# Optimization experiments

Hardware: AMD Instinct MI355X
Metric: run time of the kernel (lower is better)

## Reference

```python
import jax, jax.numpy as jnp
import numpy as np

T, B, I, H, O_FREQ, O_CTX = 1024, 32, 64, 1024, 64, 8
ALPHA = 0.1  # leak rate
G = 1.5      # chaotic gain used by init_weights


def setup_inputs() -> dict:
    key = jax.random.key(0)
    ks = jax.random.split(key, 8)
    std1 = G / np.sqrt(H)  # init_weights scaling

    def centered_normal(k, shape, std):
        w = jax.random.normal(k, shape, dtype=jnp.float32)
        return (w - w.mean()) * std

    input_sig = jax.random.normal(ks[0], (T, B, I), dtype=jnp.float32)
    rate = jax.random.uniform(ks[1], (B, H), dtype=jnp.float32, minval=-1.0, maxval=1.0)
    i2h_w = centered_normal(ks[2], (H, I), std1)
    i2h_b = jnp.zeros((H,), dtype=jnp.float32)
    h2h_w = centered_normal(ks[3], (H, H), std1)
    h2h_b = jnp.zeros((H,), dtype=jnp.float32)
    h2o_w = centered_normal(ks[4], (O_FREQ, H), std1)
    h2o_b = jnp.zeros((O_FREQ,), dtype=jnp.float32)
    h2o_ctx_w = jax.random.normal(ks[5], (O_CTX, H), dtype=jnp.float32)
    h2o_ctx_b = jnp.zeros((O_CTX,), dtype=jnp.float32)
    return {
        "input_sig": input_sig, "rate": rate,
        "i2h_w": i2h_w, "i2h_b": i2h_b,
        "h2h_w": h2h_w, "h2h_b": h2h_b,
        "h2o_w": h2o_w, "h2o_b": h2o_b,
        "h2o_ctx_w": h2o_ctx_w, "h2o_ctx_b": h2o_ctx_b,
    }


def reference(input_sig, rate, i2h_w, i2h_b, h2h_w, h2h_b,
              h2o_w, h2o_b, h2o_ctx_w, h2o_ctx_b):
    # forward_dual: leaky-tanh recurrence over T steps, then both readouts.
    # Precompute all input projections in one big GEMM: [T,B,H]
    x_proj = jnp.einsum('tbi,hi->tbh', input_sig, i2h_w) + i2h_b

    def step(r, xp):
        pre = xp + r @ h2h_w.T + h2h_b  # i2h(x_t) + h2h(r)  (no noise)
        r_new = (1.0 - ALPHA) * r + ALPHA * jnp.tanh(pre)
        return r_new, r_new

    _, rate_all = jax.lax.scan(step, rate, x_proj)  # [T,B,H]
    output = jnp.einsum('tbh,oh->tbo', rate_all, h2o_w) + h2o_b
    output_ctx = jnp.einsum('tbh,ch->tbc', rate_all, h2o_ctx_w) + h2o_ctx_b
    return (output, output_ctx, rate_all)
```

## Files before the change

kernel.cpp:

```cpp
#include <hip/hip_runtime.h>

typedef float v2f __attribute__((ext_vector_type(2)));
typedef float v4f __attribute__((ext_vector_type(4)));

constexpr int T  = 1024;
constexpr int B  = 32;
constexpr int I_ = 64;
constexpr int H  = 1024;
constexpr int OF = 64;
constexpr int OC = 8;
constexpr int NG = 16;
constexpr int NM = 16;
constexpr int CH  = 136;
constexpr int CHP = 140;
constexpr int BSTR = 8 * CHP;
constexpr long long OUT1_OFF = (long long)T * B * OF;
constexpr long long OUT2_OFF = (long long)T * B * (OF + OC);
constexpr int RING_U64 = NG * 2 * 2 * 1024;

__device__ __forceinline__ void st_agent_u64(unsigned long long* p,
                                             unsigned long long v) {
  __hip_atomic_store(p, v, __ATOMIC_RELAXED, __HIP_MEMORY_SCOPE_AGENT);
}
__device__ __forceinline__ unsigned long long
ld_agent_u64(const unsigned long long* p) {
  return __hip_atomic_load(p, __ATOMIC_RELAXED, __HIP_MEMORY_SCOPE_AGENT);
}

__global__ __launch_bounds__(512, 2) void rnn_recur(
    const float* __restrict__ input_sig, const float* __restrict__ rate0,
    const float* __restrict__ i2h_w, const float* __restrict__ i2h_b,
    const float* __restrict__ h2h_w, const float* __restrict__ h2h_b,
    float* __restrict__ rate_all, unsigned long long* __restrict__ ring)
{
  const int tid = threadIdx.x;
  const int bid = blockIdx.x;
  const int g   = bid & (NG - 1);
  const int m   = bid >> 4;
  const int l8  = tid & 7;
  const int jrel = tid >> 3;
  const int j   = m * 64 + jrel;
  const int bG  = g * 2;

  __shared__ float lds[2][BSTR];

  v2f w2[68];
#pragma unroll
  for (int q = 0; q < 68; ++q) {
    const int k = l8 * CH + q * 2;
    w2[q] = (k < H) ? *(const v2f*)(h2h_w + (long long)j * H + k)
                    : *(const v2f*)(i2h_w + (long long)j * I_ + (k - H));
  }
  const float bsum = h2h_b[j] + i2h_b[j];
  const int posj = (j / CH) * CHP + (j % CH);

  {
    const int b = tid >> 8, u4 = tid & 255;
    const int k0 = u4 * 4, c = k0 / CH, off = k0 - c * CH;
    float4 v = *(const float4*)(rate0 + (long long)(bG + b) * H + k0);
    *(float4*)&lds[b][c * CHP + off] = v;
    if (tid < 32) {
      const int b2 = tid >> 4, iq = tid & 15;
      float4 u = *(const float4*)(input_sig + (long long)(bG + b2) * I_ + iq * 4);
      *(float4*)&lds[b2][7 * CHP + 72 + iq * 4] = u;
    }
  }
  __syncthreads();

  unsigned long long* ringG = ring + (long long)g * (2 * 2 * 1024);
  const int c_  = (2 * tid) / CH;
  const int off_ = 2 * tid - c_ * CH;

  auto phase = [&](int b, int t) {
    const float* Rb = &lds[b][0];
    v2f acc2 = {0.f, 0.f};
#pragma unroll
    for (int q = 0; q < 34; ++q) {
      const v4f rv = *(const v4f*)&Rb[l8 * CHP + q * 4];
      const v2f rlo = __builtin_shufflevector(rv, rv, 0, 1);
      const v2f rhi = __builtin_shufflevector(rv, rv, 2, 3);
      acc2 = __builtin_elementwise_fma(w2[2 * q],     rlo, acc2);
      acc2 = __builtin_elementwise_fma(w2[2 * q + 1], rhi, acc2);
    }
    float acc = acc2.x + acc2.y;
    acc += __shfl_xor(acc, 4, 64);
    acc += __shfl_xor(acc, 2, 64);
    acc += __shfl_xor(acc, 1, 64);
    if (l8 == 0) {
      const float pre  = acc + bsum;
      const float rold = Rb[posj];
      const float rnew = 0.9f * rold + 0.1f * tanhf(pre);
      const unsigned long long pkt =
          ((unsigned long long)(unsigned)(t + 1) << 32) |
          (unsigned long long)__float_as_uint(rnew);
      st_agent_u64(&ringG[((long long)((t & 1) * 2 + b) << 10) + j], pkt);
      rate_all[((long long)t * B + bG + b) * H + j] = rnew;
    }
  };

  for (int t = 0; t < T; ++t) {
    unsigned long long v10 = 0, v11 = 0;
    float4 xv1;
    const bool have1 = (t > 0);
    const unsigned long long* p1 =
        &ringG[((long long)((((t - 1) & 1) * 2) + 1) << 10) + 2 * tid];
    if (have1) {
      v10 = ld_agent_u64(p1);
      v11 = ld_agent_u64(p1 + 1);
      if (tid < 16) {
        xv1 = *(const float4*)(input_sig +
            ((long long)t * B + bG + 1) * I_ + tid * 4);
      }
    }

    phase(0, t);

    if (have1) {
      const unsigned tag = (unsigned)t;
      while ((unsigned)(v10 >> 32) != tag || (unsigned)(v11 >> 32) != tag) {
        v10 = ld_agent_u64(p1);
        v11 = ld_agent_u64(p1 + 1);
      }
      *(float2*)&lds[1][c_ * CHP + off_] = make_float2(
          __uint_as_float((unsigned)v10), __uint_as_float((unsigned)v11));
      if (tid < 16) *(float4*)&lds[1][7 * CHP + 72 + tid * 4] = xv1;
    }
    __syncthreads();

    unsigned long long v00 = 0, v01 = 0;
    float4 xv0;
    const bool have0 = (t + 1 < T);
    const unsigned long long* p0 =
        &ringG[((long long)((t & 1) * 2) << 10) + 2 * tid];
    if (have0) {
      v00 = ld_agent_u64(p0);
      v01 = ld_agent_u64(p0 + 1);
      if (tid < 16) {
        xv0 = *(const float4*)(input_sig +
            ((long long)(t + 1) * B + bG) * I_ + tid * 4);
      }
    }

    phase(1, t);

    if (have0) {
      const unsigned tag = (unsigned)(t + 1);
      while ((unsigned)(v00 >> 32) != tag || (unsigned)(v01 >> 32) != tag) {
        v00 = ld_agent_u64(p0);
        v01 = ld_agent_u64(p0 + 1);
      }
      *(float2*)&lds[0][c_ * CHP + off_] = make_float2(
          __uint_as_float((unsigned)v00), __uint_as_float((unsigned)v01));
      if (tid < 16) *(float4*)&lds[0][7 * CHP + 72 + tid * 4] = xv0;
    }
    __syncthreads();
  }
}

__global__ __launch_bounds__(256) void rnn_readout(
    const float* __restrict__ rate_all,
    const float* __restrict__ h2o_w, const float* __restrict__ h2o_b,
    const float* __restrict__ h2o_ctx_w, const float* __restrict__ h2o_ctx_b,
    float* __restrict__ out0, float* __restrict__ out1)
{
  constexpr int RB = 128;
  constexpr int HC = 128;
  constexpr int SR = HC + 1;
  __shared__ float rl[RB * SR];
  __shared__ float wl[72 * SR];

  const int tid = threadIdx.x;
  const long long row0 = (long long)blockIdx.x * RB;
  const int rb = tid & 31, og = tid >> 5;

  float acc[4][9];
#pragma unroll
  for (int c = 0; c < 4; ++c)
#pragma unroll
    for (int i = 0; i < 9; ++i) acc[c][i] = 0.f;

  for (int hc = 0; hc < H / HC; ++hc) {
#pragma unroll
    for (int i = 0; i < 16; ++i) {
      const int q = i * 256 + tid;
      const int row = q >> 5, hq = q & 31;
      float4 v = *(const float4*)(rate_all + (row0 + row) * H + hc * HC + hq * 4);
      float* d = &rl[row * SR + hq * 4];
      d[0] = v.x; d[1] = v.y; d[2] = v.z; d[3] = v.w;
    }
#pragma unroll
    for (int i = 0; i < 9; ++i) {
      const int q = i * 256 + tid;
      const int o = q >> 5, hq = q & 31;
      const float* src = (o < OF) ? (h2o_w + (long long)o * H)
                                  : (h2o_ctx_w + (long long)(o - OF) * H);
      float4 v = *(const float4*)(src + hc * HC + hq * 4);
      float* d = &wl[o * SR + hq * 4];
      d[0] = v.x; d[1] = v.y; d[2] = v.z; d[3] = v.w;
    }
    __syncthreads();

#pragma unroll 4
    for (int h = 0; h < HC; ++h) {
      const float r0 = rl[(rb)      * SR + h];
      const float r1 = rl[(rb + 32) * SR + h];
      const float r2 = rl[(rb + 64) * SR + h];
      const float r3 = rl[(rb + 96) * SR + h];
#pragma unroll
      for (int i = 0; i < 9; ++i) {
        const float wv = wl[(og * 9 + i) * SR + h];
        acc[0][i] = fmaf(r0, wv, acc[0][i]);
        acc[1][i] = fmaf(r1, wv, acc[1][i]);
        acc[2][i] = fmaf(r2, wv, acc[2][i]);
        acc[3][i] = fmaf(r3, wv, acc[3][i]);
      }
    }
    __syncthreads();
  }

#pragma unroll
  for (int c = 0; c < 4; ++c) {
    const long long row = row0 + rb + 32 * c;
#pragma unroll
    for (int i = 0; i < 9; ++i) {
      const int o = og * 9 + i;
      if (o < OF) out0[row * OF + o] = acc[c][i] + h2o_b[o];
      else        out1[row * OC + (o - OF)] = acc[c][i] + h2o_ctx_b[o - OF];
    }
  }
}

extern "C" void kernel_launch(void* const* d_in, const int* in_sizes, int n_in,
                              void* d_out, int out_size, void* d_ws, size_t ws_size,
                              hipStream_t stream) {
  (void)in_sizes; (void)n_in; (void)d_ws; (void)ws_size; (void)out_size;
  const float* input_sig = (const float*)d_in[0];
  const float* rate0     = (const float*)d_in[1];
  const float* i2h_w     = (const float*)d_in[2];
  const float* i2h_b     = (const float*)d_in[3];
  const float* h2h_w     = (const float*)d_in[4];
  const float* h2h_b     = (const float*)d_in[5];
  const float* h2o_w     = (const float*)d_in[6];
  const float* h2o_b     = (const float*)d_in[7];
  const float* h2o_ctx_w = (const float*)d_in[8];
  const float* h2o_ctx_b = (const float*)d_in[9];

  float* out      = (float*)d_out;
  float* out0     = out;
  float* out1     = out + OUT1_OFF;
  float* rate_all = out + OUT2_OFF;
  unsigned long long* ring = (unsigned long long*)d_out;

  hipMemsetAsync(ring, 0, (size_t)RING_U64 * 8, stream);
  hipLaunchKernelGGL(rnn_recur, dim3(NG * NM), dim3(512), 0, stream,
                     input_sig, rate0, i2h_w, i2h_b, h2h_w, h2h_b,
                     rate_all, ring);
  hipLaunchKernelGGL(rnn_readout, dim3(256), dim3(256), 0, stream,
                     rate_all, h2o_w, h2o_b, h2o_ctx_w, h2o_ctx_b, out0, out1);
}
```

Before: 2.507 ms.

## Precompute input projection in separate kernel and shrink recurrence dot product

Adds a kernel that computes the input projection for all timesteps up front and writes it into the rate_all buffer. The recurrence then reads each value back just before overwriting it, so the per-step dot product covers only the hidden state (1024 instead of 1088 entries). This removes the per-step staging of input_sig into LDS and lets chunk indexing use power-of-two shifts and masks. The next ring load is also hoisted ahead of the first wait, and the launch bounds are relaxed. The cost is an extra kernel that writes a large intermediate, plus one global load per hidden unit per step on the latency-critical path.

Result: slower. 3.815 ms (+52.2%).

```diff
diff --git a/kernel.cpp b/kernel.cpp
--- a/kernel.cpp
+++ b/kernel.cpp
@@ -11,8 +11,8 @@
 constexpr int OC = 8;
 constexpr int NG = 16;
 constexpr int NM = 16;
-constexpr int CH  = 136;
-constexpr int CHP = 140;
+constexpr int CHK = 128;
+constexpr int CHP = 132;
 constexpr int BSTR = 8 * CHP;
 constexpr long long OUT1_OFF = (long long)T * B * OF;
 constexpr long long OUT2_OFF = (long long)T * B * (OF + OC);
@@ -27,10 +27,42 @@
   return __hip_atomic_load(p, __ATOMIC_RELAXED, __HIP_MEMORY_SCOPE_AGENT);
 }
 
-__global__ __launch_bounds__(512, 2) void rnn_recur(
-    const float* __restrict__ input_sig, const float* __restrict__ rate0,
-    const float* __restrict__ i2h_w, const float* __restrict__ i2h_b,
-    const float* __restrict__ h2h_w, const float* __restrict__ h2h_b,
+__global__ __launch_bounds__(256) void xproj_kern(
+    const float* __restrict__ input_sig, const float* __restrict__ i2h_w,
+    float* __restrict__ xp)
+{
+  __shared__ float X[8][64];
+  const int tid = threadIdx.x;
+  const long long row0 = (long long)blockIdx.x * 8;
+  if (tid < 128) {
+    const int r = tid >> 4, e = tid & 15;
+    *(float4*)&X[r][e * 4] = *(const float4*)(input_sig + (row0 + r) * I_ + e * 4);
+  }
+  __syncthreads();
+#pragma unroll
+  for (int hh = 0; hh < 4; ++hh) {
+    const int h = hh * 256 + tid;
+    const float4* wp = (const float4*)(i2h_w + (long long)h * I_);
+    float acc[8] = {0.f, 0.f, 0.f, 0.f, 0.f, 0.f, 0.f, 0.f};
+#pragma unroll
+    for (int kq = 0; kq < 16; ++kq) {
+      const float4 wv = wp[kq];
+#pragma unroll
+      for (int r = 0; r < 8; ++r) {
+        acc[r] = fmaf(wv.x, X[r][kq * 4 + 0],
+                 fmaf(wv.y, X[r][kq * 4 + 1],
+                 fmaf(wv.z, X[r][kq * 4 + 2],
+                 fmaf(wv.w, X[r][kq * 4 + 3], acc[r]))));
+      }
+    }
+#pragma unroll
+    for (int r = 0; r < 8; ++r) xp[(row0 + r) * H + h] = acc[r];
+  }
+}
+
+__global__ __launch_bounds__(512, 1) void rnn_recur(
+    const float* __restrict__ rate0, const float* __restrict__ h2h_w,
+    const float* __restrict__ i2h_b, const float* __restrict__ h2h_b,
     float* __restrict__ rate_all, unsigned long long* __restrict__ ring)
 {
   const int tid = threadIdx.x;
@@ -44,38 +76,31 @@
 
   __shared__ float lds[2][BSTR];
 
-  v2f w2[68];
-#pragma unroll
-  for (int q = 0; q < 68; ++q) {
-    const int k = l8 * CH + q * 2;
-    w2[q] = (k < H) ? *(const v2f*)(h2h_w + (long long)j * H + k)
-                    : *(const v2f*)(i2h_w + (long long)j * I_ + (k - H));
+  v2f w2[64];
+#pragma unroll
+  for (int q = 0; q < 64; ++q) {
+    w2[q] = *(const v2f*)(h2h_w + (long long)j * H + l8 * CHK + q * 2);
   }
   const float bsum = h2h_b[j] + i2h_b[j];
-  const int posj = (j / CH) * CHP + (j % CH);
+  const int posj = (j >> 7) * CHP + (j & 127);
 
   {
-    const int b = tid >> 8, u4 = tid & 255;
-    const int k0 = u4 * 4, c = k0 / CH, off = k0 - c * CH;
-    float4 v = *(const float4*)(rate0 + (long long)(bG + b) * H + k0);
-    *(float4*)&lds[b][c * CHP + off] = v;
-    if (tid < 32) {
-      const int b2 = tid >> 4, iq = tid & 15;
-      float4 u = *(const float4*)(input_sig + (long long)(bG + b2) * I_ + iq * 4);
-      *(float4*)&lds[b2][7 * CHP + 72 + iq * 4] = u;
-    }
+    const int b = tid >> 8, u = tid & 255;
+    const int k0 = u * 4, c = k0 >> 7, off = k0 & 127;
+    *(float4*)&lds[b][c * CHP + off] =
+        *(const float4*)(rate0 + (long long)(bG + b) * H + k0);
   }
   __syncthreads();
 
   unsigned long long* ringG = ring + (long long)g * (2 * 2 * 1024);
-  const int c_  = (2 * tid) / CH;
-  const int off_ = 2 * tid - c_ * CH;
-
-  auto phase = [&](int b, int t) {
+  const int c_  = tid >> 6;
+  const int off_ = 2 * tid - c_ * CHK;
+
+  auto phase = [&](int b, int t, float xp) {
     const float* Rb = &lds[b][0];
     v2f acc2 = {0.f, 0.f};
 #pragma unroll
-    for (int q = 0; q < 34; ++q) {
+    for (int q = 0; q < 32; ++q) {
       const v4f rv = *(const v4f*)&Rb[l8 * CHP + q * 4];
       const v2f rlo = __builtin_shufflevector(rv, rv, 0, 1);
       const v2f rhi = __builtin_shufflevector(rv, rv, 2, 3);
@@ -87,7 +112,7 @@
     acc += __shfl_xor(acc, 2, 64);
     acc += __shfl_xor(acc, 1, 64);
     if (l8 == 0) {
-      const float pre  = acc + bsum;
+      const float pre  = acc + xp + bsum;
       const float rold = Rb[posj];
       const float rnew = 0.9f * rold + 0.1f * tanhf(pre);
       const unsigned long long pkt =
@@ -99,21 +124,22 @@
   };
 
   for (int t = 0; t < T; ++t) {
+    const float xp0 = rate_all[((long long)t * B + bG) * H + j];
+    const float xp1 = rate_all[((long long)t * B + bG + 1) * H + j];
+
     unsigned long long v10 = 0, v11 = 0;
-    float4 xv1;
     const bool have1 = (t > 0);
     const unsigned long long* p1 =
         &ringG[((long long)((((t - 1) & 1) * 2) + 1) << 10) + 2 * tid];
-    if (have1) {
-      v10 = ld_agent_u64(p1);
-      v11 = ld_agent_u64(p1 + 1);
-      if (tid < 16) {
-        xv1 = *(const float4*)(input_sig +
-            ((long long)t * B + bG + 1) * I_ + tid * 4);
-      }
-    }
-
-    phase(0, t);
+    if (have1) { v10 = ld_agent_u64(p1); v11 = ld_agent_u64(p1 + 1); }
+
+    phase(0, t, xp0);
+
+    unsigned long long v00 = 0, v01 = 0;
+    const bool have0 = (t + 1 < T);
+    const unsigned long long* p0 =
+        &ringG[((long long)((t & 1) * 2) << 10) + 2 * tid];
+    if (have0) { v00 = ld_agent_u64(p0); v01 = ld_agent_u64(p0 + 1); }
 
     if (have1) {
       const unsigned tag = (unsigned)t;
@@ -123,25 +149,10 @@
       }
       *(float2*)&lds[1][c_ * CHP + off_] = make_float2(
           __uint_as_float((unsigned)v10), __uint_as_float((unsigned)v11));
-      if (tid < 16) *(float4*)&lds[1][7 * CHP + 72 + tid * 4] = xv1;
-    }
-    __syncthreads();
-
-    unsigned long long v00 = 0, v01 = 0;
-    float4 xv0;
-    const bool have0 = (t + 1 < T);
-    const unsigned long long* p0 =
-        &ringG[((long long)((t & 1) * 2) << 10) + 2 * tid];
-    if (have0) {
-      v00 = ld_agent_u64(p0);
-      v01 = ld_agent_u64(p0 + 1);
-      if (tid < 16) {
-        xv0 = *(const float4*)(input_sig +
-            ((long long)(t + 1) * B + bG) * I_ + tid * 4);
-      }
-    }
-
-    phase(1, t);
+    }
+    __syncthreads();
+
+    phase(1, t, xp1);
 
     if (have0) {
       const unsigned tag = (unsigned)(t + 1);
@@ -151,7 +162,6 @@
       }
       *(float2*)&lds[0][c_ * CHP + off_] = make_float2(
           __uint_as_float((unsigned)v00), __uint_as_float((unsigned)v01));
-      if (tid < 16) *(float4*)&lds[0][7 * CHP + 72 + tid * 4] = xv0;
     }
     __syncthreads();
   }
@@ -252,9 +262,10 @@
   unsigned long long* ring = (unsigned long long*)d_out;
 
   hipMemsetAsync(ring, 0, (size_t)RING_U64 * 8, stream);
+  hipLaunchKernelGGL(xproj_kern, dim3(T * B / 8), dim3(256), 0, stream,
+                     input_sig, i2h_w, rate_all);
   hipLaunchKernelGGL(rnn_recur, dim3(NG * NM), dim3(512), 0, stream,
-                     input_sig, rate0, i2h_w, i2h_b, h2h_w, h2h_b,
-                     rate_all, ring);
+                     rate0, h2h_w, i2h_b, h2h_b, rate_all, ring);
   hipLaunchKernelGGL(rnn_readout, dim3(256), dim3(256), 0, stream,
                      rate_all, h2o_w, h2o_b, h2o_ctx_w, h2o_ctx_b, out0, out1);
 }
```

## Dedicate a polling wavefront to ring probing, separate from compute warps

Applied to the files above, without the earlier changes.

Adds a ninth wavefront per block that polls the inter-block ring buffer and commits the next timestep's rates into LDS, while the eight compute wavefronts only run the matvec and meet it at raw s_barrier points. The ring grows to four slots so producers can run further ahead, and rate_all stores become agent-scope atomics. The aim is to take global polling latency off the compute path. In exchange one wave must issue 16 loads per lane per probe, occupancy drops to one block per CU, and correctness now depends on the hand-written barrier pairing between the two roles.

Result: slower. 2.890 ms (+15.3%).

```diff
diff --git a/kernel.cpp b/kernel.cpp
--- a/kernel.cpp
+++ b/kernel.cpp
@@ -16,8 +16,11 @@
 constexpr int BSTR = 8 * CHP;
 constexpr long long OUT1_OFF = (long long)T * B * OF;
 constexpr long long OUT2_OFF = (long long)T * B * (OF + OC);
-constexpr int RING_U64 = NG * 2 * 2 * 1024;
-
+constexpr int RING_U64 = NG * 4 * 2 * 1024;
+
+__device__ __forceinline__ void st_agent_f32(float* p, float v) {
+  __hip_atomic_store(p, v, __ATOMIC_RELAXED, __HIP_MEMORY_SCOPE_AGENT);
+}
 __device__ __forceinline__ void st_agent_u64(unsigned long long* p,
                                              unsigned long long v) {
   __hip_atomic_store(p, v, __ATOMIC_RELAXED, __HIP_MEMORY_SCOPE_AGENT);
@@ -27,7 +30,7 @@
   return __hip_atomic_load(p, __ATOMIC_RELAXED, __HIP_MEMORY_SCOPE_AGENT);
 }
 
-__global__ __launch_bounds__(512, 2) void rnn_recur(
+__global__ __launch_bounds__(576, 1) void rnn_recur(
     const float* __restrict__ input_sig, const float* __restrict__ rate0,
     const float* __restrict__ i2h_w, const float* __restrict__ i2h_b,
     const float* __restrict__ h2h_w, const float* __restrict__ h2h_b,
@@ -36,25 +39,11 @@
   const int tid = threadIdx.x;
   const int bid = blockIdx.x;
   const int g   = bid & (NG - 1);
-  const int m   = bid >> 4;
-  const int l8  = tid & 7;
-  const int jrel = tid >> 3;
-  const int j   = m * 64 + jrel;
   const int bG  = g * 2;
 
   __shared__ float lds[2][BSTR];
 
-  v2f w2[68];
-#pragma unroll
-  for (int q = 0; q < 68; ++q) {
-    const int k = l8 * CH + q * 2;
-    w2[q] = (k < H) ? *(const v2f*)(h2h_w + (long long)j * H + k)
-                    : *(const v2f*)(i2h_w + (long long)j * I_ + (k - H));
-  }
-  const float bsum = h2h_b[j] + i2h_b[j];
-  const int posj = (j / CH) * CHP + (j % CH);
-
-  {
+  if (tid < 512) {
     const int b = tid >> 8, u4 = tid & 255;
     const int k0 = u4 * 4, c = k0 / CH, off = k0 - c * CH;
     float4 v = *(const float4*)(rate0 + (long long)(bG + b) * H + k0);
@@ -67,93 +56,112 @@
   }
   __syncthreads();
 
-  unsigned long long* ringG = ring + (long long)g * (2 * 2 * 1024);
-  const int c_  = (2 * tid) / CH;
-  const int off_ = 2 * tid - c_ * CH;
-
-  auto phase = [&](int b, int t) {
-    const float* Rb = &lds[b][0];
-    v2f acc2 = {0.f, 0.f};
-#pragma unroll
-    for (int q = 0; q < 34; ++q) {
-      const v4f rv = *(const v4f*)&Rb[l8 * CHP + q * 4];
-      const v2f rlo = __builtin_shufflevector(rv, rv, 0, 1);
-      const v2f rhi = __builtin_shufflevector(rv, rv, 2, 3);
-      acc2 = __builtin_elementwise_fma(w2[2 * q],     rlo, acc2);
-      acc2 = __builtin_elementwise_fma(w2[2 * q + 1], rhi, acc2);
-    }
-    float acc = acc2.x + acc2.y;
-    acc += __shfl_xor(acc, 4, 64);
-    acc += __shfl_xor(acc, 2, 64);
-    acc += __shfl_xor(acc, 1, 64);
-    if (l8 == 0) {
-      const float pre  = acc + bsum;
-      const float rold = Rb[posj];
-      const float rnew = 0.9f * rold + 0.1f * tanhf(pre);
-      const unsigned long long pkt =
-          ((unsigned long long)(unsigned)(t + 1) << 32) |
-          (unsigned long long)__float_as_uint(rnew);
-      st_agent_u64(&ringG[((long long)((t & 1) * 2 + b) << 10) + j], pkt);
-      rate_all[((long long)t * B + bG + b) * H + j] = rnew;
-    }
-  };
-
-  for (int t = 0; t < T; ++t) {
-    unsigned long long v10 = 0, v11 = 0;
-    float4 xv1;
-    const bool have1 = (t > 0);
-    const unsigned long long* p1 =
-        &ringG[((long long)((((t - 1) & 1) * 2) + 1) << 10) + 2 * tid];
-    if (have1) {
-      v10 = ld_agent_u64(p1);
-      v11 = ld_agent_u64(p1 + 1);
-      if (tid < 16) {
-        xv1 = *(const float4*)(input_sig +
-            ((long long)t * B + bG + 1) * I_ + tid * 4);
-      }
-    }
-
-    phase(0, t);
-
-    if (have1) {
-      const unsigned tag = (unsigned)t;
-      while ((unsigned)(v10 >> 32) != tag || (unsigned)(v11 >> 32) != tag) {
-        v10 = ld_agent_u64(p1);
-        v11 = ld_agent_u64(p1 + 1);
-      }
-      *(float2*)&lds[1][c_ * CHP + off_] = make_float2(
-          __uint_as_float((unsigned)v10), __uint_as_float((unsigned)v11));
-      if (tid < 16) *(float4*)&lds[1][7 * CHP + 72 + tid * 4] = xv1;
-    }
-    __syncthreads();
-
-    unsigned long long v00 = 0, v01 = 0;
-    float4 xv0;
-    const bool have0 = (t + 1 < T);
-    const unsigned long long* p0 =
-        &ringG[((long long)((t & 1) * 2) << 10) + 2 * tid];
-    if (have0) {
-      v00 = ld_agent_u64(p0);
-      v01 = ld_agent_u64(p0 + 1);
-      if (tid < 16) {
-        xv0 = *(const float4*)(input_sig +
-            ((long long)(t + 1) * B + bG) * I_ + tid * 4);
-      }
-    }
-
-    phase(1, t);
-
-    if (have0) {
-      const unsigned tag = (unsigned)(t + 1);
-      while ((unsigned)(v00 >> 32) != tag || (unsigned)(v01 >> 32) != tag) {
-        v00 = ld_agent_u64(p0);
-        v01 = ld_agent_u64(p0 + 1);
-      }
-      *(float2*)&lds[0][c_ * CHP + off_] = make_float2(
-          __uint_as_float((unsigned)v00), __uint_as_float((unsigned)v01));
-      if (tid < 16) *(float4*)&lds[0][7 * CHP + 72 + tid * 4] = xv0;
-    }
-    __syncthreads();
+  unsigned long long* ringG = ring + (long long)g * (4 * 2 * 1024);
+
+  if (tid < 512) {
+    const int m    = bid >> 4;
+    const int l8   = tid & 7;
+    const int jrel = tid >> 3;
+    const int j    = m * 64 + jrel;
+
+    v2f w2[68];
+#pragma unroll
+    for (int q = 0; q < 68; ++q) {
+      const int k = l8 * CH + q * 2;
+      w2[q] = (k < H) ? *(const v2f*)(h2h_w + (long long)j * H + k)
+                      : *(const v2f*)(i2h_w + (long long)j * I_ + (k - H));
+    }
+    const float bsum = h2h_b[j] + i2h_b[j];
+    const int posj = (j / CH) * CHP + (j % CH);
+
+    auto phase = [&](int b, int t) {
+      const float* Rb = &lds[b][0];
+      v2f acc2 = {0.f, 0.f};
+#pragma unroll
+      for (int q = 0; q < 34; ++q) {
+        const v4f rv = *(const v4f*)&Rb[l8 * CHP + q * 4];
+        const v2f rlo = __builtin_shufflevector(rv, rv, 0, 1);
+        const v2f rhi = __builtin_shufflevector(rv, rv, 2, 3);
+        acc2 = __builtin_elementwise_fma(w2[2 * q],     rlo, acc2);
+        acc2 = __builtin_elementwise_fma(w2[2 * q + 1], rhi, acc2);
+      }
+      float acc = acc2.x + acc2.y;
+      acc += __shfl_xor(acc, 4, 64);
+      acc += __shfl_xor(acc, 2, 64);
+      acc += __shfl_xor(acc, 1, 64);
+      if (l8 == 0) {
+        const float pre  = acc + bsum;
+        const float rold = Rb[posj];
+        const float rnew = 0.9f * rold + 0.1f * tanhf(pre);
+        const unsigned long long pkt =
+            ((unsigned long long)(unsigned)(t + 1) << 32) |
+            (unsigned long long)__float_as_uint(rnew);
+        st_agent_u64(&ringG[((long long)((t & 3) * 2 + b) << 10) + j], pkt);
+        st_agent_f32(&rate_all[((long long)t * B + bG + b) * H + j], rnew);
+      }
+    };
+
+    for (int t = 0; t < T; ++t) {
+      phase(0, t);
+      asm volatile("s_waitcnt lgkmcnt(0)\n\ts_barrier" ::: "memory");
+      phase(1, t);
+      asm volatile("s_waitcnt lgkmcnt(0)\n\ts_barrier" ::: "memory");
+    }
+  } else {
+    const int l = tid - 512;
+
+    auto probe_commit = [&](const unsigned long long* p, unsigned tag,
+                            int dst, const float* xsrc) {
+      float4 xv;
+      if (l < 16) xv = *(const float4*)(xsrc + l * 4);
+      unsigned long long v0, v1, v2, v3, v4, v5, v6, v7;
+      unsigned long long v8, v9, va, vb, vc, vd, ve, vf;
+      bool ok;
+      do {
+        v0 = ld_agent_u64(p + 0);  v1 = ld_agent_u64(p + 1);
+        v2 = ld_agent_u64(p + 2);  v3 = ld_agent_u64(p + 3);
+        v4 = ld_agent_u64(p + 4);  v5 = ld_agent_u64(p + 5);
+        v6 = ld_agent_u64(p + 6);  v7 = ld_agent_u64(p + 7);
+        v8 = ld_agent_u64(p + 8);  v9 = ld_agent_u64(p + 9);
+        va = ld_agent_u64(p + 10); vb = ld_agent_u64(p + 11);
+        vc = ld_agent_u64(p + 12); vd = ld_agent_u64(p + 13);
+        ve = ld_agent_u64(p + 14); vf = ld_agent_u64(p + 15);
+        ok =  ((unsigned)(v0 >> 32) == tag) & ((unsigned)(v1 >> 32) == tag)
+            & ((unsigned)(v2 >> 32) == tag) & ((unsigned)(v3 >> 32) == tag)
+            & ((unsigned)(v4 >> 32) == tag) & ((unsigned)(v5 >> 32) == tag)
+            & ((unsigned)(v6 >> 32) == tag) & ((unsigned)(v7 >> 32) == tag)
+            & ((unsigned)(v8 >> 32) == tag) & ((unsigned)(v9 >> 32) == tag)
+            & ((unsigned)(va >> 32) == tag) & ((unsigned)(vb >> 32) == tag)
+            & ((unsigned)(vc >> 32) == tag) & ((unsigned)(vd >> 32) == tag)
+            & ((unsigned)(ve >> 32) == tag) & ((unsigned)(vf >> 32) == tag);
+      } while (!ok);
+      unsigned long long vv[16] = {v0,v1,v2,v3,v4,v5,v6,v7,
+                                   v8,v9,va,vb,vc,vd,ve,vf};
+#pragma unroll
+      for (int i = 0; i < 16; ++i) {
+        const int row = 16 * l + i;
+        lds[dst][(row / CH) * CHP + (row % CH)] =
+            __uint_as_float((unsigned)vv[i]);
+      }
+      if (l < 16) *(float4*)&lds[dst][7 * CHP + 72 + l * 4] = xv;
+    };
+
+    for (int t = 0; t < T; ++t) {
+      if (t >= 1) {
+        probe_commit(
+            &ringG[((long long)((((t - 1) & 3) * 2) + 1) << 10) + 16 * l],
+            (unsigned)t, 1,
+            input_sig + ((long long)t * B + bG + 1) * I_);
+      }
+      asm volatile("s_waitcnt lgkmcnt(0)\n\ts_barrier" ::: "memory");
+      if (t + 1 < T) {
+        probe_commit(
+            &ringG[((long long)((t & 3) * 2) << 10) + 16 * l],
+            (unsigned)(t + 1), 0,
+            input_sig + ((long long)(t + 1) * B + bG) * I_);
+      }
+      asm volatile("s_waitcnt lgkmcnt(0)\n\ts_barrier" ::: "memory");
+    }
   }
 }
 
@@ -252,7 +260,7 @@
   unsigned long long* ring = (unsigned long long*)d_out;
 
   hipMemsetAsync(ring, 0, (size_t)RING_U64 * 8, stream);
-  hipLaunchKernelGGL(rnn_recur, dim3(NG * NM), dim3(512), 0, stream,
+  hipLaunchKernelGGL(rnn_recur, dim3(NG * NM), dim3(576), 0, stream,
                      input_sig, rate0, i2h_w, i2h_b, h2h_w, h2h_b,
                      rate_all, ring);
   hipLaunchKernelGGL(rnn_readout, dim3(256), dim3(256), 0, stream,
```
